# Kernel tuning notes

Measured on AMD Instinct MI355X. Metric: run time of the kernel, lower is better.

The kernel has to match this reference:

```python
import jax, jax.numpy as jnp
import numpy as np

INPUT_SIZE = 1024
HIDDEN = 2048
NUM_LAYERS = 4
TIME_STEPS = 16
BATCH = 64


def setup_inputs() -> dict:
    key = jax.random.key(0)
    ks = jax.random.split(key, 20)
    s = 1.0 / np.sqrt(HIDDEN)
    u = lambda k, shape: jax.random.uniform(k, shape, jnp.float32, -s, s)
    inp = {
        "x": jax.random.normal(ks[0], (BATCH, TIME_STEPS, INPUT_SIZE), jnp.float32),
        # layer 0 (input size 1024)
        "w_ih0": u(ks[1], (4 * HIDDEN, INPUT_SIZE)),
        "w_hh0": u(ks[2], (4 * HIDDEN, HIDDEN)),
        "b_ih0": u(ks[3], (4 * HIDDEN,)),
        "b_hh0": u(ks[4], (4 * HIDDEN,)),
        # layers 1..3 (input size HIDDEN), stacked on leading axis
        "w_ih_r": u(ks[5], (NUM_LAYERS - 1, 4 * HIDDEN, HIDDEN)),
        "w_hh_r": u(ks[6], (NUM_LAYERS - 1, 4 * HIDDEN, HIDDEN)),
        "b_ih_r": u(ks[7], (NUM_LAYERS - 1, 4 * HIDDEN)),
        "b_hh_r": u(ks[8], (NUM_LAYERS - 1, 4 * HIDDEN)),
    }
    return inp


def _lstm_layer(x, w_ih, w_hh, b_ih, b_hh):
    """x: [B, T, D_in] -> [B, T, H]. PyTorch gate order: i, f, g, o."""
    B = x.shape[0]
    # precompute input projections for all timesteps: [T, B, 4H]
    xi = jnp.einsum('btd,gd->tbg', x, w_ih) + b_ih + b_hh

    def step(carry, xt):
        h, c = carry  # [B, H]
        gates = xt + h @ w_hh.T  # [B, 4H]
        i, f, g, o = jnp.split(gates, 4, axis=-1)
        i = jax.nn.sigmoid(i)
        f = jax.nn.sigmoid(f)
        g = jnp.tanh(g)
        o = jax.nn.sigmoid(o)
        c = f * c + i * g
        h = o * jnp.tanh(c)
        return (h, c), h

    h0 = jnp.zeros((B, HIDDEN), x.dtype)
    c0 = jnp.zeros((B, HIDDEN), x.dtype)
    _, hs = jax.lax.scan(step, (h0, c0), xi)  # hs: [T, B, H]
    return jnp.transpose(hs, (1, 0, 2))  # [B, T, H]


def reference(x, w_ih0, w_hh0, b_ih0, b_hh0, w_ih_r, w_hh_r, b_ih_r, b_hh_r):
    # Stepping all layers one timestep at a time (as in the torch code) is
    # mathematically identical to processing the full sequence layer by layer.
    h = _lstm_layer(x, w_ih0, w_hh0, b_ih0, b_hh0)
    for l in range(NUM_LAYERS - 1):
        h = _lstm_layer(h, w_ih_r[l], w_hh_r[l], b_ih_r[l], b_hh_r[l])
    # original returns a list of 16 [B,1,H] outputs; concatenated -> [B,T,H]
    return h
```

## Files before the change

### kernel.cpp

```cpp
#include <hip/hip_runtime.h>
#include <stdint.h>

#define B_ 64
#define T_ 16
#define D0 1024
#define H_ 2048
#define G4 8192
#define NB 256

typedef unsigned short u16;
typedef unsigned long long u64;
typedef __attribute__((ext_vector_type(4))) float f32x4;
typedef __attribute__((ext_vector_type(8))) short bf16x8;

__device__ __forceinline__ u16 f2bf(float f) {
  unsigned int u = __builtin_bit_cast(unsigned int, f);
  unsigned int r = (u + 0x7FFFu + ((u >> 16) & 1u)) >> 16;
  return (u16)r;
}
__device__ __forceinline__ short f2bf_s(float f) { return (short)f2bf(f); }

__device__ __forceinline__ void gld_lds16(const void* g, void* l) {
  __builtin_amdgcn_global_load_lds(
      (const __attribute__((address_space(1))) void*)g,
      (__attribute__((address_space(3))) void*)l, 16, 0, 0);
}

__device__ __forceinline__ bf16x8 frag_from_u4(uint4 q) {
  return __builtin_bit_cast(bf16x8, q);
}

__global__ __launch_bounds__(256) void k_f32_to_bf16(
    const float* __restrict__ src, u16* __restrict__ dst, int n8) {
  int i = blockIdx.x * 256 + threadIdx.x;
  int stride = gridDim.x * 256;
  const float4* s = (const float4*)src;
  uint4* d = (uint4*)dst;
  for (; i < n8; i += stride) {
    float4 a = s[2 * i], b = s[2 * i + 1];
    uint4 o;
    o.x = f2bf(a.x) | ((unsigned)f2bf(a.y) << 16);
    o.y = f2bf(a.z) | ((unsigned)f2bf(a.w) << 16);
    o.z = f2bf(b.x) | ((unsigned)f2bf(b.y) << 16);
    o.w = f2bf(b.z) | ((unsigned)f2bf(b.w) << 16);
    d[i] = o;
  }
}

__global__ __launch_bounds__(256) void k_bias(
    const float* __restrict__ bih0, const float* __restrict__ bhh0,
    const float* __restrict__ bihr, const float* __restrict__ bhhr,
    float* __restrict__ bias) {
  int i = blockIdx.x * 256 + threadIdx.x;
  if (i >= 4 * G4) return;
  int l = i >> 13, j = i & (G4 - 1);
  float a = (l == 0) ? bih0[j] : bihr[(l - 1) * G4 + j];
  float b = (l == 0) ? bhh0[j] : bhhr[(l - 1) * G4 + j];
  bias[i] = a + b;
}

__global__ __launch_bounds__(256) void k_stage_x(
    const float* __restrict__ x, uint4* __restrict__ A16) {
  int i = blockIdx.x * 256 + threadIdx.x;
  if (i >= T_ * (D0 / 8) * B_) return;
  int chunk = i & 127;
  int r = i >> 7;
  int b = r & (B_ - 1), t = r >> 6;
  const float4* s = (const float4*)(x + ((size_t)(b * T_ + t)) * D0 + chunk * 8);
  float4 a0 = s[0], a1 = s[1];
  uint4 o;
  o.x = f2bf(a0.x) | ((unsigned)f2bf(a0.y) << 16);
  o.y = f2bf(a0.z) | ((unsigned)f2bf(a0.w) << 16);
  o.z = f2bf(a1.x) | ((unsigned)f2bf(a1.y) << 16);
  o.w = f2bf(a1.z) | ((unsigned)f2bf(a1.w) << 16);
  A16[((size_t)t * 128 + chunk) * 64 + b] = o;
}

__global__ __launch_bounds__(256) void k_gemm_xi(
    const u16* __restrict__ A, const u16* __restrict__ W,
    const float* __restrict__ bias, float* __restrict__ C, int K, int CH) {
  __shared__ __align__(16) u16 sA[128 * 32];
  __shared__ __align__(16) u16 sB[128 * 32];
  const int tid = threadIdx.x;
  const int wave = tid >> 6;
  const int lane = tid & 63;
  const int m0 = blockIdx.y * 128;
  const int n0 = blockIdx.x * 128;
  const int wr = wave >> 1, wc = wave & 1;
  const int lr = lane & 15;
  const int kc = (lane >> 4) * 8;
  const int rowA = tid >> 2, colk = (tid & 3) * 8;

  f32x4 acc[4][4] = {};

  for (int k0 = 0; k0 < K; k0 += 32) {
#pragma unroll
    for (int iss = 0; iss < 2; ++iss) {
      int row = m0 + iss * 64 + rowA;
      int tt = row >> 6, bb = row & 63;
      int chunk = (k0 + colk) >> 3;
      gld_lds16(A + ((((size_t)tt * CH + chunk) * 64 + bb) << 3),
                sA + (iss * 64 + wave * 16) * 32);
      gld_lds16(W + (size_t)(n0 + iss * 64 + rowA) * K + k0 + colk,
                sB + (iss * 64 + wave * 16) * 32);
    }
    __syncthreads();
    bf16x8 a[4], b[4];
#pragma unroll
    for (int m = 0; m < 4; ++m)
      a[m] = *(const bf16x8*)&sA[(wr * 64 + m * 16 + lr) * 32 + kc];
#pragma unroll
    for (int n = 0; n < 4; ++n)
      b[n] = *(const bf16x8*)&sB[(wc * 64 + n * 16 + lr) * 32 + kc];
#pragma unroll
    for (int m = 0; m < 4; ++m)
#pragma unroll
      for (int n = 0; n < 4; ++n)
        acc[m][n] = __builtin_amdgcn_mfma_f32_16x16x32_bf16(a[m], b[n], acc[m][n], 0, 0, 0);
    __syncthreads();
  }

#pragma unroll
  for (int n = 0; n < 4; ++n) {
    int col = n0 + wc * 64 + n * 16 + lr;
    float bv = bias[col];
#pragma unroll
    for (int m = 0; m < 4; ++m) {
      int row0 = m0 + wr * 64 + m * 16 + ((lane >> 4) << 2);
      int t = row0 >> 6, b0 = row0 & 63;
      float4 v;
      v.x = acc[m][n][0] + bv;
      v.y = acc[m][n][1] + bv;
      v.z = acc[m][n][2] + bv;
      v.w = acc[m][n][3] + bv;
      *(float4*)&C[((size_t)t * G4 + col) * B_ + b0] = v;
    }
  }
}

__global__ __launch_bounds__(256, 1) void k_lstm_seq(
    const float* __restrict__ whh,
    const float* __restrict__ xi,
    u16* __restrict__ hfr,
    float* __restrict__ out32,
    unsigned* __restrict__ flg,
    const float* __restrict__ wih_next,
    const float* __restrict__ bias_next,
    float* __restrict__ xi_next) {
  __builtin_amdgcn_fence(__ATOMIC_ACQUIRE, "agent");

  __shared__ float red[4][64][33];
  __shared__ unsigned harr[64][4];
  __shared__ float hfar[64][9];
  __shared__ float bbuf[32];

  const int tid = threadIdx.x;
  const int wave = tid >> 6;
  const int lane = tid & 63;
  const int lr = lane & 15;
  const int kc = lane >> 4;
  const int jb = blockIdx.x * 8;
  const bool has_next = (wih_next != nullptr);

  bf16x8 warr[2][16];
#pragma unroll
  for (int n = 0; n < 2; ++n) {
    int row = n * 16 + lr;
    int grow = (row >> 3) * H_ + jb + (row & 7);
    const float* wp = whh + (size_t)grow * H_ + wave * 512 + kc * 8;
#pragma unroll
    for (int kk = 0; kk < 16; ++kk) {
      float4 f0 = *(const float4*)(wp + kk * 32);
      float4 f1 = *(const float4*)(wp + kk * 32 + 4);
      bf16x8 w;
      w[0] = f2bf_s(f0.x); w[1] = f2bf_s(f0.y); w[2] = f2bf_s(f0.z); w[3] = f2bf_s(f0.w);
      w[4] = f2bf_s(f1.x); w[5] = f2bf_s(f1.y); w[6] = f2bf_s(f1.z); w[7] = f2bf_s(f1.w);
      warr[n][kk] = w;
    }
  }

  bf16x8 wnarr[2][16];
  if (has_next) {
#pragma unroll
    for (int n = 0; n < 2; ++n) {
      int row = n * 16 + lr;
      int grow = (row >> 3) * H_ + jb + (row & 7);
      const float* wp = wih_next + (size_t)grow * H_ + wave * 512 + kc * 8;
#pragma unroll
      for (int kk = 0; kk < 16; ++kk) {
        float4 f0 = *(const float4*)(wp + kk * 32);
        float4 f1 = *(const float4*)(wp + kk * 32 + 4);
        bf16x8 w;
        w[0] = f2bf_s(f0.x); w[1] = f2bf_s(f0.y); w[2] = f2bf_s(f0.z); w[3] = f2bf_s(f0.w);
        w[4] = f2bf_s(f1.x); w[5] = f2bf_s(f1.y); w[6] = f2bf_s(f1.z); w[7] = f2bf_s(f1.w);
        wnarr[n][kk] = w;
      }
    }
    if (tid < 32) bbuf[tid] = bias_next[(tid >> 3) * H_ + jb + (tid & 7)];
  }
  __syncthreads();

  const uint4* const H16 = (const uint4*)hfr;
  u64* const hq = (u64*)hfr;

  const int cb = tid & 63;
  const int cp = tid >> 6;
  const int j0 = 2 * cp, j1 = 2 * cp + 1;
  float cst0 = 0.f, cst1 = 0.f;

  auto xi_writeback = [&](int tt) {
    __syncthreads();
#pragma unroll
    for (int j = 0; j < 8; ++j) {
      int e = tid + 256 * j;
      int b = e & 63, r = e >> 6;
      float v = red[0][b][r] + red[1][b][r] + red[2][b][r] + red[3][b][r] + bbuf[r];
      xi_next[((size_t)tt * G4 + (r >> 3) * H_ + jb + (r & 7)) * (size_t)B_ + b] = v;
    }
    __syncthreads();
  };

  for (int t = 0; t < T_; ++t) {
    float xv0[4], xv1[4];
    {
      const float* xp = xi + (size_t)t * G4 * B_ + (size_t)(jb + j0) * B_ + cb;
#pragma unroll
      for (int g = 0; g < 4; ++g) {
        xv0[g] = xp[(size_t)g * H_ * B_];
        xv1[g] = xp[(size_t)g * H_ * B_ + B_];
      }
    }

    f32x4 acc[4][2] = {};
    f32x4 facc[4][2] = {};
    if (t > 0) {
      const unsigned* fp = flg + (size_t)(t - 1) * 256 + wave * 64 + lane;
      while (__hip_atomic_load(fp, __ATOMIC_RELAXED,
                               __HIP_MEMORY_SCOPE_SYSTEM) == 0u)
        __builtin_amdgcn_s_sleep(1);
      asm volatile("" ::: "memory");

      const size_t base = ((size_t)(t - 1) * 256 + wave * 64 + kc) * 64 + lr;
      uint4 pre[2][4];
#pragma unroll
      for (int d = 0; d < 2; ++d)
#pragma unroll
        for (int m = 0; m < 4; ++m)
          pre[d][m] = H16[base + (size_t)d * 256 + m * 16];
#pragma unroll
      for (int kk = 0; kk < 16; ++kk) {
        const int slot = kk & 1;
        bf16x8 af[4];
#pragma unroll
        for (int m = 0; m < 4; ++m)
          af[m] = frag_from_u4(pre[slot][m]);
        if (kk + 2 < 16) {
#pragma unroll
          for (int m = 0; m < 4; ++m)
            pre[slot][m] = H16[base + (size_t)(kk + 2) * 256 + m * 16];
        }
#pragma unroll
        for (int m = 0; m < 4; ++m) {
          acc[m][0] = __builtin_amdgcn_mfma_f32_16x16x32_bf16(af[m], warr[0][kk], acc[m][0], 0, 0, 0);
          acc[m][1] = __builtin_amdgcn_mfma_f32_16x16x32_bf16(af[m], warr[1][kk], acc[m][1], 0, 0, 0);
        }
        if (has_next) {
#pragma unroll
          for (int m = 0; m < 4; ++m) {
            facc[m][0] = __builtin_amdgcn_mfma_f32_16x16x32_bf16(af[m], wnarr[0][kk], facc[m][0], 0, 0, 0);
            facc[m][1] = __builtin_amdgcn_mfma_f32_16x16x32_bf16(af[m], wnarr[1][kk], facc[m][1], 0, 0, 0);
          }
        }
      }
    }

#pragma unroll
    for (int m = 0; m < 4; ++m)
#pragma unroll
      for (int n = 0; n < 2; ++n)
#pragma unroll
        for (int j = 0; j < 4; ++j)
          red[wave][m * 16 + kc * 4 + j][n * 16 + lr] = acc[m][n][j];
    __syncthreads();

    {
      float s00 = red[0][cb][j0]      + red[1][cb][j0]      + red[2][cb][j0]      + red[3][cb][j0];
      float s01 = red[0][cb][8 + j0]  + red[1][cb][8 + j0]  + red[2][cb][8 + j0]  + red[3][cb][8 + j0];
      float s02 = red[0][cb][16 + j0] + red[1][cb][16 + j0] + red[2][cb][16 + j0] + red[3][cb][16 + j0];
      float s03 = red[0][cb][24 + j0] + red[1][cb][24 + j0] + red[2][cb][24 + j0] + red[3][cb][24 + j0];
      float iv = s00 + xv0[0];
      float fv = s01 + xv0[1];
      float gv = s02 + xv0[2];
      float ov = s03 + xv0[3];
      iv = 1.f / (1.f + expf(-iv));
      fv = 1.f / (1.f + expf(-fv));
      gv = tanhf(gv);
      ov = 1.f / (1.f + expf(-ov));
      cst0 = fv * cst0 + iv * gv;
      float hv0 = ov * tanhf(cst0);

      float s10 = red[0][cb][j1]      + red[1][cb][j1]      + red[2][cb][j1]      + red[3][cb][j1];
      float s11 = red[0][cb][8 + j1]  + red[1][cb][8 + j1]  + red[2][cb][8 + j1]  + red[3][cb][8 + j1];
      float s12 = red[0][cb][16 + j1] + red[1][cb][16 + j1] + red[2][cb][16 + j1] + red[3][cb][16 + j1];
      float s13 = red[0][cb][24 + j1] + red[1][cb][24 + j1] + red[2][cb][24 + j1] + red[3][cb][24 + j1];
      float iv1 = s10 + xv1[0];
      float fv1 = s11 + xv1[1];
      float gv1 = s12 + xv1[2];
      float ov1 = s13 + xv1[3];
      iv1 = 1.f / (1.f + expf(-iv1));
      fv1 = 1.f / (1.f + expf(-fv1));
      gv1 = tanhf(gv1);
      ov1 = 1.f / (1.f + expf(-ov1));
      cst1 = fv1 * cst1 + iv1 * gv1;
      float hv1 = ov1 * tanhf(cst1);

      harr[cb][cp] = (unsigned)f2bf(hv0) | ((unsigned)f2bf(hv1) << 16);
      hfar[cb][j0] = hv0;
      hfar[cb][j1] = hv1;
    }
    __syncthreads();

    if (tid < B_) {
      u64 q0 = (u64)harr[tid][0] | ((u64)harr[tid][1] << 32);
      u64 q1 = (u64)harr[tid][2] | ((u64)harr[tid][3] << 32);
      u64* hp = hq + ((((size_t)t * 256 + blockIdx.x) * 64 + tid) << 1);
      __hip_atomic_store(hp, q0, __ATOMIC_RELAXED, __HIP_MEMORY_SCOPE_SYSTEM);
      __hip_atomic_store(hp + 1, q1, __ATOMIC_RELAXED, __HIP_MEMORY_SCOPE_SYSTEM);
      if (out32 != nullptr) {
        float* op = out32 + ((size_t)tid * T_ + t) * H_ + jb;
        float4 v0, v1;
        v0.x = hfar[tid][0]; v0.y = hfar[tid][1]; v0.z = hfar[tid][2]; v0.w = hfar[tid][3];
        v1.x = hfar[tid][4]; v1.y = hfar[tid][5]; v1.z = hfar[tid][6]; v1.w = hfar[tid][7];
        *(float4*)op = v0;
        *(float4*)(op + 4) = v1;
      }
    }
    if (tid == 0) {
      asm volatile("s_waitcnt vmcnt(0)" ::: "memory");
      __hip_atomic_store(flg + (size_t)t * 256 + blockIdx.x, 1u,
                         __ATOMIC_RELAXED, __HIP_MEMORY_SCOPE_SYSTEM);
    }

    if (has_next && t > 0) {
      __syncthreads();
#pragma unroll
      for (int m = 0; m < 4; ++m)
#pragma unroll
        for (int n = 0; n < 2; ++n)
#pragma unroll
          for (int j = 0; j < 4; ++j)
            red[wave][m * 16 + kc * 4 + j][n * 16 + lr] = facc[m][n][j];
      xi_writeback(t - 1);
    }
  }

  if (has_next) {
    const unsigned* fp = flg + (size_t)15 * 256 + wave * 64 + lane;
    while (__hip_atomic_load(fp, __ATOMIC_RELAXED,
                             __HIP_MEMORY_SCOPE_SYSTEM) == 0u)
      __builtin_amdgcn_s_sleep(1);
    asm volatile("" ::: "memory");

    f32x4 facc[4][2] = {};
    const size_t base = ((size_t)15 * 256 + wave * 64 + kc) * 64 + lr;
    uint4 pre[2][4];
#pragma unroll
    for (int d = 0; d < 2; ++d)
#pragma unroll
      for (int m = 0; m < 4; ++m)
        pre[d][m] = H16[base + (size_t)d * 256 + m * 16];
#pragma unroll
    for (int kk = 0; kk < 16; ++kk) {
      const int slot = kk & 1;
      bf16x8 af[4];
#pragma unroll
      for (int m = 0; m < 4; ++m)
        af[m] = frag_from_u4(pre[slot][m]);
      if (kk + 2 < 16) {
#pragma unroll
        for (int m = 0; m < 4; ++m)
          pre[slot][m] = H16[base + (size_t)(kk + 2) * 256 + m * 16];
      }
#pragma unroll
      for (int m = 0; m < 4; ++m) {
        facc[m][0] = __builtin_amdgcn_mfma_f32_16x16x32_bf16(af[m], wnarr[0][kk], facc[m][0], 0, 0, 0);
        facc[m][1] = __builtin_amdgcn_mfma_f32_16x16x32_bf16(af[m], wnarr[1][kk], facc[m][1], 0, 0, 0);
      }
    }
    __syncthreads();
#pragma unroll
    for (int m = 0; m < 4; ++m)
#pragma unroll
      for (int n = 0; n < 2; ++n)
#pragma unroll
        for (int j = 0; j < 4; ++j)
          red[wave][m * 16 + kc * 4 + j][n * 16 + lr] = facc[m][n][j];
    xi_writeback(15);
  }
}

extern "C" void kernel_launch(void* const* d_in, const int* in_sizes, int n_in,
                              void* d_out, int out_size, void* d_ws, size_t ws_size,
                              hipStream_t stream) {
  const float* x    = (const float*)d_in[0];
  const float* wih0 = (const float*)d_in[1];
  const float* whh0 = (const float*)d_in[2];
  const float* bih0 = (const float*)d_in[3];
  const float* bhh0 = (const float*)d_in[4];
  const float* wihr = (const float*)d_in[5];
  const float* whhr = (const float*)d_in[6];
  const float* bihr = (const float*)d_in[7];
  const float* bhhr = (const float*)d_in[8];
  float* out = (float*)d_out;

  char* ws = (char*)d_ws;
  size_t off = 0;
  auto alloc = [&](size_t bytes) -> void* {
    void* p = ws + off;
    off += (bytes + 255) & ~(size_t)255;
    return p;
  };
  u16*      wih_b = (u16*)alloc((size_t)G4 * D0 * 2);
  float*    bias  = (float*)alloc(4ull * G4 * 4);
  float*    xiA   = (float*)alloc((size_t)T_ * B_ * G4 * 4);
  float*    xiB   = (float*)alloc((size_t)T_ * B_ * G4 * 4);
  u16*      Ax    = (u16*)alloc((size_t)T_ * B_ * D0 * 2);
  u16*      bufA  = (u16*)alloc((size_t)T_ * B_ * H_ * 2);
  u16*      bufB  = (u16*)alloc((size_t)T_ * B_ * H_ * 2);
  unsigned* flags = (unsigned*)alloc(4ull * 16 * 256 * sizeof(unsigned));

  auto cgrid = [](int n8) { int g = (n8 + 255) / 256; return g > 8192 ? 8192 : g; };

  hipMemsetAsync(flags, 0, 4ull * 16 * 256 * sizeof(unsigned), stream);

  int n8 = (G4 * D0) / 8;
  k_f32_to_bf16<<<cgrid(n8), 256, 0, stream>>>(wih0, wih_b, n8);

  k_bias<<<(4 * G4 + 255) / 256, 256, 0, stream>>>(bih0, bhh0, bihr, bhhr, bias);
  k_stage_x<<<(T_ * (D0 / 8) * B_ + 255) / 256, 256, 0, stream>>>(x, (uint4*)Ax);

  {
    dim3 g(G4 / 128, (T_ * B_) / 128);
    k_gemm_xi<<<g, 256, 0, stream>>>(Ax, wih_b, bias, xiA, D0, D0 / 8);
  }

  for (int l = 0; l < 4; ++l) {
    const float* whh_l = (l == 0) ? whh0 : (whhr + (size_t)(l - 1) * G4 * H_);
    u16* hbuf = (l & 1) ? bufB : bufA;
    float* o32 = (l == 3) ? out : nullptr;
    float* xi_in  = (l & 1) ? xiB : xiA;
    float* xi_out = (l & 1) ? xiA : xiB;
    const float* wih_next = (l < 3) ? (wihr + (size_t)l * G4 * H_) : nullptr;
    const float* bias_next = bias + (size_t)((l + 1) & 3) * G4;

    k_lstm_seq<<<NB, 256, 0, stream>>>(whh_l, xi_in, hbuf, o32,
                                       flags + (size_t)l * 16 * 256,
                                       wih_next, bias_next, xi_out);
  }
}
```

Before: 628.7 us.

## Fuse four per-layer LSTM launches into one persistent kernel

Replaces the four per-layer k_lstm_seq launches with a single persistent k_lstm_all kernel that loops over layers internally. Each layer gets its own hidden-state buffer and flag region, so no cross-layer reuse hazards arise. Timestep 0, which has no recurrent term, now runs before the next layer's recurrent and input weights are loaded and converted to bf16, hiding part of that load. The prefetch depth of hidden-state fragments is also raised from 2 to 4 slots. This removes kernel launch boundaries and drain/fill gaps between layers, at the cost of more register pressure and reliance on all 256 blocks being co-resident.

```diff
diff --git a/kernel.cpp b/kernel.cpp
--- a/kernel.cpp
+++ b/kernel.cpp
@@ -138,15 +138,16 @@
   }
 }
 
-__global__ __launch_bounds__(256, 1) void k_lstm_seq(
-    const float* __restrict__ whh,
-    const float* __restrict__ xi,
-    u16* __restrict__ hfr,
+__global__ __launch_bounds__(256, 1) void k_lstm_all(
+    const float* __restrict__ whh0,
+    const float* __restrict__ whhr,
+    const float* __restrict__ wihr,
+    float* __restrict__ xiA,
+    float* __restrict__ xiB,
+    u16* __restrict__ hbase,
     float* __restrict__ out32,
-    unsigned* __restrict__ flg,
-    const float* __restrict__ wih_next,
-    const float* __restrict__ bias_next,
-    float* __restrict__ xi_next) {
+    const float* __restrict__ bias,
+    unsigned* __restrict__ flags) {
   __builtin_amdgcn_fence(__ATOMIC_ACQUIRE, "agent");
 
   __shared__ float red[4][64][33];
@@ -160,32 +161,182 @@
   const int lr = lane & 15;
   const int kc = lane >> 4;
   const int jb = blockIdx.x * 8;
-  const bool has_next = (wih_next != nullptr);
+
+  const int cb = tid & 63;
+  const int cp = tid >> 6;
+  const int j0 = 2 * cp, j1 = 2 * cp + 1;
 
   bf16x8 warr[2][16];
-#pragma unroll
-  for (int n = 0; n < 2; ++n) {
-    int row = n * 16 + lr;
-    int grow = (row >> 3) * H_ + jb + (row & 7);
-    const float* wp = whh + (size_t)grow * H_ + wave * 512 + kc * 8;
-#pragma unroll
-    for (int kk = 0; kk < 16; ++kk) {
-      float4 f0 = *(const float4*)(wp + kk * 32);
-      float4 f1 = *(const float4*)(wp + kk * 32 + 4);
-      bf16x8 w;
-      w[0] = f2bf_s(f0.x); w[1] = f2bf_s(f0.y); w[2] = f2bf_s(f0.z); w[3] = f2bf_s(f0.w);
-      w[4] = f2bf_s(f1.x); w[5] = f2bf_s(f1.y); w[6] = f2bf_s(f1.z); w[7] = f2bf_s(f1.w);
-      warr[n][kk] = w;
-    }
-  }
-
   bf16x8 wnarr[2][16];
-  if (has_next) {
+
+  for (int l = 0; l < 4; ++l) {
+    const bool has_next = (l < 3);
+    const float* whh_l = (l == 0) ? whh0 : whhr + (size_t)(l - 1) * G4 * H_;
+    const float* wih_next = has_next ? wihr + (size_t)l * G4 * H_ : nullptr;
+    const float* xi_in = (l & 1) ? xiB : xiA;
+    float* xi_next = (l & 1) ? xiA : xiB;
+    u16* hfr = hbase + (size_t)l * T_ * 256 * 64 * 8;
+    const uint4* H16 = (const uint4*)hfr;
+    u64* hq = (u64*)hfr;
+    unsigned* flg = flags + (size_t)l * 16 * 256;
+    float* o32 = (l == 3) ? out32 : nullptr;
+    const float* bias_next = bias + (size_t)((l + 1) & 3) * G4;
+
+    float cst0 = 0.f, cst1 = 0.f;
+
+    auto xi_writeback = [&](int tt) {
+      __syncthreads();
+#pragma unroll
+      for (int j = 0; j < 8; ++j) {
+        int e = tid + 256 * j;
+        int b = e & 63, r = e >> 6;
+        float v = red[0][b][r] + red[1][b][r] + red[2][b][r] + red[3][b][r] + bbuf[r];
+        xi_next[((size_t)tt * G4 + (r >> 3) * H_ + jb + (r & 7)) * (size_t)B_ + b] = v;
+      }
+      __syncthreads();
+    };
+
+    auto do_step = [&](int t) {
+      float xv0[4], xv1[4];
+      {
+        const float* xp = xi_in + (size_t)t * G4 * B_ + (size_t)(jb + j0) * B_ + cb;
+#pragma unroll
+        for (int g = 0; g < 4; ++g) {
+          xv0[g] = xp[(size_t)g * H_ * B_];
+          xv1[g] = xp[(size_t)g * H_ * B_ + B_];
+        }
+      }
+
+      f32x4 acc[4][2] = {};
+      f32x4 facc[4][2] = {};
+      if (t > 0) {
+        const unsigned* fp = flg + (size_t)(t - 1) * 256 + wave * 64 + lane;
+        while (__hip_atomic_load(fp, __ATOMIC_RELAXED,
+                                 __HIP_MEMORY_SCOPE_SYSTEM) == 0u)
+          __builtin_amdgcn_s_sleep(1);
+        asm volatile("" ::: "memory");
+
+        const size_t base = ((size_t)(t - 1) * 256 + wave * 64 + kc) * 64 + lr;
+        uint4 pre[4][4];
+#pragma unroll
+        for (int d = 0; d < 4; ++d)
+#pragma unroll
+          for (int m = 0; m < 4; ++m)
+            pre[d][m] = H16[base + (size_t)d * 256 + m * 16];
+#pragma unroll
+        for (int kk = 0; kk < 16; ++kk) {
+          const int slot = kk & 3;
+          bf16x8 af[4];
+#pragma unroll
+          for (int m = 0; m < 4; ++m)
+            af[m] = frag_from_u4(pre[slot][m]);
+          if (kk + 4 < 16) {
+#pragma unroll
+            for (int m = 0; m < 4; ++m)
+              pre[slot][m] = H16[base + (size_t)(kk + 4) * 256 + m * 16];
+          }
+#pragma unroll
+          for (int m = 0; m < 4; ++m) {
+            acc[m][0] = __builtin_amdgcn_mfma_f32_16x16x32_bf16(af[m], warr[0][kk], acc[m][0], 0, 0, 0);
+            acc[m][1] = __builtin_amdgcn_mfma_f32_16x16x32_bf16(af[m], warr[1][kk], acc[m][1], 0, 0, 0);
+          }
+          if (has_next) {
+#pragma unroll
+            for (int m = 0; m < 4; ++m) {
+              facc[m][0] = __builtin_amdgcn_mfma_f32_16x16x32_bf16(af[m], wnarr[0][kk], facc[m][0], 0, 0, 0);
+              facc[m][1] = __builtin_amdgcn_mfma_f32_16x16x32_bf16(af[m], wnarr[1][kk], facc[m][1], 0, 0, 0);
+            }
+          }
+        }
+      }
+
+#pragma unroll
+      for (int m = 0; m < 4; ++m)
+#pragma unroll
+        for (int n = 0; n < 2; ++n)
+#pragma unroll
+          for (int j = 0; j < 4; ++j)
+            red[wave][m * 16 + kc * 4 + j][n * 16 + lr] = acc[m][n][j];
+      __syncthreads();
+
+      {
+        float s00 = red[0][cb][j0]      + red[1][cb][j0]      + red[2][cb][j0]      + red[3][cb][j0];
+        float s01 = red[0][cb][8 + j0]  + red[1][cb][8 + j0]  + red[2][cb][8 + j0]  + red[3][cb][8 + j0];
+        float s02 = red[0][cb][16 + j0] + red[1][cb][16 + j0] + red[2][cb][16 + j0] + red[3][cb][16 + j0];
+        float s03 = red[0][cb][24 + j0] + red[1][cb][24 + j0] + red[2][cb][24 + j0] + red[3][cb][24 + j0];
+        float iv = s00 + xv0[0];
+        float fv = s01 + xv0[1];
+        float gv = s02 + xv0[2];
+        float ov = s03 + xv0[3];
+        iv = 1.f / (1.f + expf(-iv));
+        fv = 1.f / (1.f + expf(-fv));
+        gv = tanhf(gv);
+        ov = 1.f / (1.f + expf(-ov));
+        cst0 = fv * cst0 + iv * gv;
+        float hv0 = ov * tanhf(cst0);
+
+        float s10 = red[0][cb][j1]      + red[1][cb][j1]      + red[2][cb][j1]      + red[3][cb][j1];
+        float s11 = red[0][cb][8 + j1]  + red[1][cb][8 + j1]  + red[2][cb][8 + j1]  + red[3][cb][8 + j1];
+        float s12 = red[0][cb][16 + j1] + red[1][cb][16 + j1] + red[2][cb][16 + j1] + red[3][cb][16 + j1];
+        float s13 = red[0][cb][24 + j1] + red[1][cb][24 + j1] + red[2][cb][24 + j1] + red[3][cb][24 + j1];
+        float iv1 = s10 + xv1[0];
+        float fv1 = s11 + xv1[1];
+        float gv1 = s12 + xv1[2];
+        float ov1 = s13 + xv1[3];
+        iv1 = 1.f / (1.f + expf(-iv1));
+        fv1 = 1.f / (1.f + expf(-fv1));
+        gv1 = tanhf(gv1);
+        ov1 = 1.f / (1.f + expf(-ov1));
+        cst1 = fv1 * cst1 + iv1 * gv1;
+        float hv1 = ov1 * tanhf(cst1);
+
+        harr[cb][cp] = (unsigned)f2bf(hv0) | ((unsigned)f2bf(hv1) << 16);
+        hfar[cb][j0] = hv0;
+        hfar[cb][j1] = hv1;
+      }
+      __syncthreads();
+
+      if (tid < B_) {
+        u64 q0 = (u64)harr[tid][0] | ((u64)harr[tid][1] << 32);
+        u64 q1 = (u64)harr[tid][2] | ((u64)harr[tid][3] << 32);
+        u64* hp = hq + ((((size_t)t * 256 + blockIdx.x) * 64 + tid) << 1);
+        __hip_atomic_store(hp, q0, __ATOMIC_RELAXED, __HIP_MEMORY_SCOPE_SYSTEM);
+        __hip_atomic_store(hp + 1, q1, __ATOMIC_RELAXED, __HIP_MEMORY_SCOPE_SYSTEM);
+        if (o32 != nullptr) {
+          float* op = o32 + ((size_t)tid * T_ + t) * H_ + jb;
+          float4 v0, v1;
+          v0.x = hfar[tid][0]; v0.y = hfar[tid][1]; v0.z = hfar[tid][2]; v0.w = hfar[tid][3];
+          v1.x = hfar[tid][4]; v1.y = hfar[tid][5]; v1.z = hfar[tid][6]; v1.w = hfar[tid][7];
+          *(float4*)op = v0;
+          *(float4*)(op + 4) = v1;
+        }
+      }
+      if (tid == 0) {
+        asm volatile("s_waitcnt vmcnt(0)" ::: "memory");
+        __hip_atomic_store(flg + (size_t)t * 256 + blockIdx.x, 1u,
+                           __ATOMIC_RELAXED, __HIP_MEMORY_SCOPE_SYSTEM);
+      }
+
+      if (has_next && t > 0) {
+        __syncthreads();
+#pragma unroll
+        for (int m = 0; m < 4; ++m)
+#pragma unroll
+          for (int n = 0; n < 2; ++n)
+#pragma unroll
+            for (int j = 0; j < 4; ++j)
+              red[wave][m * 16 + kc * 4 + j][n * 16 + lr] = facc[m][n][j];
+        xi_writeback(t - 1);
+      }
+    };
+
+    do_step(0);
+
 #pragma unroll
     for (int n = 0; n < 2; ++n) {
       int row = n * 16 + lr;
       int grow = (row >> 3) * H_ + jb + (row & 7);
-      const float* wp = wih_next + (size_t)grow * H_ + wave * 512 + kc * 8;
+      const float* wp = whh_l + (size_t)grow * H_ + wave * 512 + kc * 8;
 #pragma unroll
       for (int kk = 0; kk < 16; ++kk) {
         float4 f0 = *(const float4*)(wp + kk * 32);
@@ -193,54 +344,40 @@
         bf16x8 w;
         w[0] = f2bf_s(f0.x); w[1] = f2bf_s(f0.y); w[2] = f2bf_s(f0.z); w[3] = f2bf_s(f0.w);
         w[4] = f2bf_s(f1.x); w[5] = f2bf_s(f1.y); w[6] = f2bf_s(f1.z); w[7] = f2bf_s(f1.w);
-        wnarr[n][kk] = w;
+        warr[n][kk] = w;
       }
     }
-    if (tid < 32) bbuf[tid] = bias_next[(tid >> 3) * H_ + jb + (tid & 7)];
-  }
-  __syncthreads();
-
-  const uint4* const H16 = (const uint4*)hfr;
-  u64* const hq = (u64*)hfr;
-
-  const int cb = tid & 63;
-  const int cp = tid >> 6;
-  const int j0 = 2 * cp, j1 = 2 * cp + 1;
-  float cst0 = 0.f, cst1 = 0.f;
-
-  auto xi_writeback = [&](int tt) {
-    __syncthreads();
-#pragma unroll
-    for (int j = 0; j < 8; ++j) {
-      int e = tid + 256 * j;
-      int b = e & 63, r = e >> 6;
-      float v = red[0][b][r] + red[1][b][r] + red[2][b][r] + red[3][b][r] + bbuf[r];
-      xi_next[((size_t)tt * G4 + (r >> 3) * H_ + jb + (r & 7)) * (size_t)B_ + b] = v;
+    if (has_next) {
+#pragma unroll
+      for (int n = 0; n < 2; ++n) {
+        int row = n * 16 + lr;
+        int grow = (row >> 3) * H_ + jb + (row & 7);
+        const float* wp = wih_next + (size_t)grow * H_ + wave * 512 + kc * 8;
+#pragma unroll
+        for (int kk = 0; kk < 16; ++kk) {
+          float4 f0 = *(const float4*)(wp + kk * 32);
+          float4 f1 = *(const float4*)(wp + kk * 32 + 4);
+          bf16x8 w;
+          w[0] = f2bf_s(f0.x); w[1] = f2bf_s(f0.y); w[2] = f2bf_s(f0.z); w[3] = f2bf_s(f0.w);
+          w[4] = f2bf_s(f1.x); w[5] = f2bf_s(f1.y); w[6] = f2bf_s(f1.z); w[7] = f2bf_s(f1.w);
+          wnarr[n][kk] = w;
+        }
+      }
+      if (tid < 32) bbuf[tid] = bias_next[(tid >> 3) * H_ + jb + (tid & 7)];
     }
     __syncthreads();
-  };
-
-  for (int t = 0; t < T_; ++t) {
-    float xv0[4], xv1[4];
-    {
-      const float* xp = xi + (size_t)t * G4 * B_ + (size_t)(jb + j0) * B_ + cb;
-#pragma unroll
-      for (int g = 0; g < 4; ++g) {
-        xv0[g] = xp[(size_t)g * H_ * B_];
-        xv1[g] = xp[(size_t)g * H_ * B_ + B_];
-      }
-    }
-
-    f32x4 acc[4][2] = {};
-    f32x4 facc[4][2] = {};
-    if (t > 0) {
-      const unsigned* fp = flg + (size_t)(t - 1) * 256 + wave * 64 + lane;
+
+    for (int t = 1; t < T_; ++t) do_step(t);
+
+    if (has_next) {
+      const unsigned* fp = flg + (size_t)15 * 256 + wave * 64 + lane;
       while (__hip_atomic_load(fp, __ATOMIC_RELAXED,
                                __HIP_MEMORY_SCOPE_SYSTEM) == 0u)
         __builtin_amdgcn_s_sleep(1);
       asm volatile("" ::: "memory");
 
-      const size_t base = ((size_t)(t - 1) * 256 + wave * 64 + kc) * 64 + lr;
+      f32x4 facc[4][2] = {};
+      const size_t base = ((size_t)15 * 256 + wave * 64 + kc) * 64 + lr;
       uint4 pre[2][4];
 #pragma unroll
       for (int d = 0; d < 2; ++d)
@@ -261,87 +398,10 @@
         }
 #pragma unroll
         for (int m = 0; m < 4; ++m) {
-          acc[m][0] = __builtin_amdgcn_mfma_f32_16x16x32_bf16(af[m], warr[0][kk], acc[m][0], 0, 0, 0);
-          acc[m][1] = __builtin_amdgcn_mfma_f32_16x16x32_bf16(af[m], warr[1][kk], acc[m][1], 0, 0, 0);
-        }
-        if (has_next) {
-#pragma unroll
-          for (int m = 0; m < 4; ++m) {
-            facc[m][0] = __builtin_amdgcn_mfma_f32_16x16x32_bf16(af[m], wnarr[0][kk], facc[m][0], 0, 0, 0);
-            facc[m][1] = __builtin_amdgcn_mfma_f32_16x16x32_bf16(af[m], wnarr[1][kk], facc[m][1], 0, 0, 0);
-          }
-        }
-      }
-    }
-
-#pragma unroll
-    for (int m = 0; m < 4; ++m)
-#pragma unroll
-      for (int n = 0; n < 2; ++n)
-#pragma unroll
-        for (int j = 0; j < 4; ++j)
-          red[wave][m * 16 + kc * 4 + j][n * 16 + lr] = acc[m][n][j];
-    __syncthreads();
-
-    {
-      float s00 = red[0][cb][j0]      + red[1][cb][j0]      + red[2][cb][j0]      + red[3][cb][j0];
-      float s01 = red[0][cb][8 + j0]  + red[1][cb][8 + j0]  + red[2][cb][8 + j0]  + red[3][cb][8 + j0];
-      float s02 = red[0][cb][16 + j0] + red[1][cb][16 + j0] + red[2][cb][16 + j0] + red[3][cb][16 + j0];
-      float s03 = red[0][cb][24 + j0] + red[1][cb][24 + j0] + red[2][cb][24 + j0] + red[3][cb][24 + j0];
-      float iv = s00 + xv0[0];
-      float fv = s01 + xv0[1];
-      float gv = s02 + xv0[2];
-      float ov = s03 + xv0[3];
-      iv = 1.f / (1.f + expf(-iv));
-      fv = 1.f / (1.f + expf(-fv));
-      gv = tanhf(gv);
-      ov = 1.f / (1.f + expf(-ov));
-      cst0 = fv * cst0 + iv * gv;
-      float hv0 = ov * tanhf(cst0);
-
-      float s10 = red[0][cb][j1]      + red[1][cb][j1]      + red[2][cb][j1]      + red[3][cb][j1];
-      float s11 = red[0][cb][8 + j1]  + red[1][cb][8 + j1]  + red[2][cb][8 + j1]  + red[3][cb][8 + j1];
-      float s12 = red[0][cb][16 + j1] + red[1][cb][16 + j1] + red[2][cb][16 + j1] + red[3][cb][16 + j1];
-      float s13 = red[0][cb][24 + j1] + red[1][cb][24 + j1] + red[2][cb][24 + j1] + red[3][cb][24 + j1];
-      float iv1 = s10 + xv1[0];
-      float fv1 = s11 + xv1[1];
-      float gv1 = s12 + xv1[2];
-      float ov1 = s13 + xv1[3];
-      iv1 = 1.f / (1.f + expf(-iv1));
-      fv1 = 1.f / (1.f + expf(-fv1));
-      gv1 = tanhf(gv1);
-      ov1 = 1.f / (1.f + expf(-ov1));
-      cst1 = fv1 * cst1 + iv1 * gv1;
-      float hv1 = ov1 * tanhf(cst1);
-
-      harr[cb][cp] = (unsigned)f2bf(hv0) | ((unsigned)f2bf(hv1) << 16);
-      hfar[cb][j0] = hv0;
-      hfar[cb][j1] = hv1;
-    }
-    __syncthreads();
-
-    if (tid < B_) {
-      u64 q0 = (u64)harr[tid][0] | ((u64)harr[tid][1] << 32);
-      u64 q1 = (u64)harr[tid][2] | ((u64)harr[tid][3] << 32);
-      u64* hp = hq + ((((size_t)t * 256 + blockIdx.x) * 64 + tid) << 1);
-      __hip_atomic_store(hp, q0, __ATOMIC_RELAXED, __HIP_MEMORY_SCOPE_SYSTEM);
-      __hip_atomic_store(hp + 1, q1, __ATOMIC_RELAXED, __HIP_MEMORY_SCOPE_SYSTEM);
-      if (out32 != nullptr) {
-        float* op = out32 + ((size_t)tid * T_ + t) * H_ + jb;
-        float4 v0, v1;
-        v0.x = hfar[tid][0]; v0.y = hfar[tid][1]; v0.z = hfar[tid][2]; v0.w = hfar[tid][3];
-        v1.x = hfar[tid][4]; v1.y = hfar[tid][5]; v1.z = hfar[tid][6]; v1.w = hfar[tid][7];
-        *(float4*)op = v0;
-        *(float4*)(op + 4) = v1;
-      }
-    }
-    if (tid == 0) {
-      asm volatile("s_waitcnt vmcnt(0)" ::: "memory");
-      __hip_atomic_store(flg + (size_t)t * 256 + blockIdx.x, 1u,
-                         __ATOMIC_RELAXED, __HIP_MEMORY_SCOPE_SYSTEM);
-    }
-
-    if (has_next && t > 0) {
+          facc[m][0] = __builtin_amdgcn_mfma_f32_16x16x32_bf16(af[m], wnarr[0][kk], facc[m][0], 0, 0, 0);
+          facc[m][1] = __builtin_amdgcn_mfma_f32_16x16x32_bf16(af[m], wnarr[1][kk], facc[m][1], 0, 0, 0);
+        }
+      }
       __syncthreads();
 #pragma unroll
       for (int m = 0; m < 4; ++m)
@@ -350,52 +410,8 @@
 #pragma unroll
           for (int j = 0; j < 4; ++j)
             red[wave][m * 16 + kc * 4 + j][n * 16 + lr] = facc[m][n][j];
-      xi_writeback(t - 1);
+      xi_writeback(15);
     }
-  }
-
-  if (has_next) {
-    const unsigned* fp = flg + (size_t)15 * 256 + wave * 64 + lane;
-    while (__hip_atomic_load(fp, __ATOMIC_RELAXED,
-                             __HIP_MEMORY_SCOPE_SYSTEM) == 0u)
-      __builtin_amdgcn_s_sleep(1);
-    asm volatile("" ::: "memory");
-
-    f32x4 facc[4][2] = {};
-    const size_t base = ((size_t)15 * 256 + wave * 64 + kc) * 64 + lr;
-    uint4 pre[2][4];
-#pragma unroll
-    for (int d = 0; d < 2; ++d)
-#pragma unroll
-      for (int m = 0; m < 4; ++m)
-        pre[d][m] = H16[base + (size_t)d * 256 + m * 16];
-#pragma unroll
-    for (int kk = 0; kk < 16; ++kk) {
-      const int slot = kk & 1;
-      bf16x8 af[4];
-#pragma unroll
-      for (int m = 0; m < 4; ++m)
-        af[m] = frag_from_u4(pre[slot][m]);
-      if (kk + 2 < 16) {
-#pragma unroll
-        for (int m = 0; m < 4; ++m)
-          pre[slot][m] = H16[base + (size_t)(kk + 2) * 256 + m * 16];
-      }
-#pragma unroll
-      for (int m = 0; m < 4; ++m) {
-        facc[m][0] = __builtin_amdgcn_mfma_f32_16x16x32_bf16(af[m], wnarr[0][kk], facc[m][0], 0, 0, 0);
-        facc[m][1] = __builtin_amdgcn_mfma_f32_16x16x32_bf16(af[m], wnarr[1][kk], facc[m][1], 0, 0, 0);
-      }
-    }
-    __syncthreads();
-#pragma unroll
-    for (int m = 0; m < 4; ++m)
-#pragma unroll
-      for (int n = 0; n < 2; ++n)
-#pragma unroll
-        for (int j = 0; j < 4; ++j)
-          red[wave][m * 16 + kc * 4 + j][n * 16 + lr] = facc[m][n][j];
-    xi_writeback(15);
   }
 }
 
@@ -425,8 +441,7 @@
   float*    xiA   = (float*)alloc((size_t)T_ * B_ * G4 * 4);
   float*    xiB   = (float*)alloc((size_t)T_ * B_ * G4 * 4);
   u16*      Ax    = (u16*)alloc((size_t)T_ * B_ * D0 * 2);
-  u16*      bufA  = (u16*)alloc((size_t)T_ * B_ * H_ * 2);
-  u16*      bufB  = (u16*)alloc((size_t)T_ * B_ * H_ * 2);
+  u16*      hbase = (u16*)alloc(4ull * T_ * B_ * H_ * 2);
   unsigned* flags = (unsigned*)alloc(4ull * 16 * 256 * sizeof(unsigned));
 
   auto cgrid = [](int n8) { int g = (n8 + 255) / 256; return g > 8192 ? 8192 : g; };
@@ -444,17 +459,6 @@
     k_gemm_xi<<<g, 256, 0, stream>>>(Ax, wih_b, bias, xiA, D0, D0 / 8);
   }
 
-  for (int l = 0; l < 4; ++l) {
-    const float* whh_l = (l == 0) ? whh0 : (whhr + (size_t)(l - 1) * G4 * H_);
-    u16* hbuf = (l & 1) ? bufB : bufA;
-    float* o32 = (l == 3) ? out : nullptr;
-    float* xi_in  = (l & 1) ? xiB : xiA;
-    float* xi_out = (l & 1) ? xiA : xiB;
-    const float* wih_next = (l < 3) ? (wihr + (size_t)l * G4 * H_) : nullptr;
-    const float* bias_next = bias + (size_t)((l + 1) & 3) * G4;
-
-    k_lstm_seq<<<NB, 256, 0, stream>>>(whh_l, xi_in, hbuf, o32,
-                                       flags + (size_t)l * 16 * 256,
-                                       wih_next, bias_next, xi_out);
-  }
-}
+  k_lstm_all<<<NB, 256, 0, stream>>>(whh0, whhr, wihr, xiA, xiB, hbase, out,
+                                     bias, flags);
+}
```

Result: slower. 708.5 us (+12.7%).

## Split flag wait into two halves to overlap recurrent matmul with producers

Applied to the files above, without the earlier changes.

The wait on producer flags for the previous timestep's hidden state is split in two. The first half of the K-chunks is waited on and consumed before the second half's flags are polled, so MFMA work can start while later producers are still finishing. This adds a second spin-wait and an extra prefetch restart, and it relies on the flag-to-chunk mapping (lanes 0-31 covering kk 0-7) being correct.

```diff
diff --git a/kernel.cpp b/kernel.cpp
--- a/kernel.cpp
+++ b/kernel.cpp
@@ -234,21 +234,64 @@
     f32x4 acc[4][2] = {};
     f32x4 facc[4][2] = {};
     if (t > 0) {
-      const unsigned* fp = flg + (size_t)(t - 1) * 256 + wave * 64 + lane;
-      while (__hip_atomic_load(fp, __ATOMIC_RELAXED,
-                               __HIP_MEMORY_SCOPE_SYSTEM) == 0u)
-        __builtin_amdgcn_s_sleep(1);
-      asm volatile("" ::: "memory");
-
+      const unsigned* fbase = flg + (size_t)(t - 1) * 256 + wave * 64;
       const size_t base = ((size_t)(t - 1) * 256 + wave * 64 + kc) * 64 + lr;
       uint4 pre[2][4];
+
+      if (lane < 32) {
+        const unsigned* fp = fbase + lane;
+        while (__hip_atomic_load(fp, __ATOMIC_RELAXED,
+                                 __HIP_MEMORY_SCOPE_SYSTEM) == 0u)
+          __builtin_amdgcn_s_sleep(1);
+      }
+      asm volatile("" ::: "memory");
+
 #pragma unroll
       for (int d = 0; d < 2; ++d)
 #pragma unroll
         for (int m = 0; m < 4; ++m)
           pre[d][m] = H16[base + (size_t)d * 256 + m * 16];
 #pragma unroll
-      for (int kk = 0; kk < 16; ++kk) {
+      for (int kk = 0; kk < 8; ++kk) {
+        const int slot = kk & 1;
+        bf16x8 af[4];
+#pragma unroll
+        for (int m = 0; m < 4; ++m)
+          af[m] = frag_from_u4(pre[slot][m]);
+        if (kk + 2 < 8) {
+#pragma unroll
+          for (int m = 0; m < 4; ++m)
+            pre[slot][m] = H16[base + (size_t)(kk + 2) * 256 + m * 16];
+        }
+#pragma unroll
+        for (int m = 0; m < 4; ++m) {
+          acc[m][0] = __builtin_amdgcn_mfma_f32_16x16x32_bf16(af[m], warr[0][kk], acc[m][0], 0, 0, 0);
+          acc[m][1] = __builtin_amdgcn_mfma_f32_16x16x32_bf16(af[m], warr[1][kk], acc[m][1], 0, 0, 0);
+        }
+        if (has_next) {
+#pragma unroll
+          for (int m = 0; m < 4; ++m) {
+            facc[m][0] = __builtin_amdgcn_mfma_f32_16x16x32_bf16(af[m], wnarr[0][kk], facc[m][0], 0, 0, 0);
+            facc[m][1] = __builtin_amdgcn_mfma_f32_16x16x32_bf16(af[m], wnarr[1][kk], facc[m][1], 0, 0, 0);
+          }
+        }
+      }
+
+      if (lane < 32) {
+        const unsigned* fp = fbase + 32 + lane;
+        while (__hip_atomic_load(fp, __ATOMIC_RELAXED,
+                                 __HIP_MEMORY_SCOPE_SYSTEM) == 0u)
+          __builtin_amdgcn_s_sleep(1);
+      }
+      asm volatile("" ::: "memory");
+
+#pragma unroll
+      for (int d = 0; d < 2; ++d)
+#pragma unroll
+        for (int m = 0; m < 4; ++m)
+          pre[d][m] = H16[base + (size_t)(8 + d) * 256 + m * 16];
+#pragma unroll
+      for (int kk = 8; kk < 16; ++kk) {
         const int slot = kk & 1;
         bf16x8 af[4];
 #pragma unroll
```

New measurement: 626.8 us. No clear change (-0.3%).
